# Optimization experiments

Hardware: AMD Instinct MI355X
Metric: run time of the kernel (lower is better)

The kernel has to match this reference:

```python
import jax, jax.numpy as jnp
import numpy as np

N, T, F = 4096, 10, 512
NHID, NCLASS = 64, 16


def setup_inputs() -> dict:
    key = jax.random.key(0)
    k1, k2, k3, k4, k5, k6 = jax.random.split(key, 6)
    feats = jax.random.normal(k1, (N, T, F), dtype=jnp.float32)
    adj = jax.random.uniform(k2, (T, N, N), dtype=jnp.float32)
    # GCNConv parameters (glorot-ish scale)
    W1 = jax.random.normal(k3, (F, NHID), dtype=jnp.float32) * (1.0 / np.sqrt(F))
    b1 = jnp.zeros((NHID,), dtype=jnp.float32)
    W2 = jax.random.normal(k4, (NHID, NCLASS), dtype=jnp.float32) * (1.0 / np.sqrt(NHID))
    b2 = jnp.zeros((NCLASS,), dtype=jnp.float32)
    lam = jnp.float32(0.2)
    return {"feats": feats, "adj": adj, "lam": lam,
            "W1": W1, "b1": b1, "W2": W2, "b2": b2}


def _fold_adj(adj, lam):
    # tf.foldl: prev = adj[0]; prev = (1-lam)*prev + lam*adj[t] for t=1..T-1
    def step(prev, a):
        return (1.0 - lam) * prev + lam * a, None
    folded, _ = jax.lax.scan(step, adj[0], adj[1:])
    # '0 * lam +' term from the original (a no-op numerically, kept for fidelity)
    return 0.0 * lam + folded


def reference(feats, adj, lam, W1, b1, W2, b2):
    A = _fold_adj(adj, lam)                      # [N, N]
    x = feats[:, -1, :]                          # [N, F] last snapshot features
    # GCNConv 1: relu(A @ (X W1) + b1)
    h = jax.nn.relu(A @ (x @ W1) + b1)           # [N, NHID]
    # dropout is identity in eval mode (training=None)
    # GCNConv 2: softmax(A @ (H W2) + b2)
    logits = A @ (h @ W2) + b2                   # [N, NCLASS]
    return jax.nn.softmax(logits, axis=-1)
```

## Files before the change

### kernel.cpp

```cpp
#include <hip/hip_runtime.h>
#include <stdint.h>

#define NN 4096
#define TT 10
#define FF 512
#define NHID 64
#define NCLASS 16

#define G1_BM 128
#define G1_BK 64
#define G1_SPLITS 8
#define G2_BM 64
#define G2_BK 64
#define G2_SPLITS 16

__global__ void fold_k(const float4* __restrict__ adj, float4* __restrict__ A,
                       const float* __restrict__ lam_p) {
    const float lam = lam_p[0];
    const float w = 1.0f - lam;
    const int64_t slice = (int64_t)NN * NN / 4;
    const int64_t stride = (int64_t)gridDim.x * blockDim.x;
    for (int64_t i = (int64_t)blockIdx.x * blockDim.x + threadIdx.x; i < slice; i += stride) {
        float4 v = adj[i];
#pragma unroll
        for (int t = 1; t < TT; ++t) {
            float4 a = adj[(int64_t)t * slice + i];
            v.x = w * v.x + lam * a.x;
            v.y = w * v.y + lam * a.y;
            v.z = w * v.z + lam * a.z;
            v.w = w * v.w + lam * a.w;
        }
        A[i] = v;
    }
}

__global__ __launch_bounds__(64) void xw1_k(const float* __restrict__ feats,
                                            const float* __restrict__ W1,
                                            float* __restrict__ XW1T) {
    __shared__ float xs[FF];
    const int n = blockIdx.x;
    const int k = threadIdx.x;
    const float4* xr4 = (const float4*)(feats + ((int64_t)n * TT + (TT - 1)) * FF);
    float4* xs4 = (float4*)xs;
#pragma unroll
    for (int f = k; f < FF / 4; f += 64) xs4[f] = xr4[f];
    __syncthreads();
    float acc = 0.0f;
#pragma unroll 8
    for (int f = 0; f < FF; ++f) acc = fmaf(xs[f], W1[f * NHID + k], acc);
    XW1T[(int64_t)k * NN + n] = acc;
}

__global__ __launch_bounds__(256) void gemm1_k(const float* __restrict__ A,
                                               const float* __restrict__ XW1T,
                                               float* __restrict__ Y1P) {
    __shared__ float As[G1_BM][G1_BK + 4];
    __shared__ float Bs[NHID][G1_BK + 4];
    const int t = threadIdx.x;
    const int r0 = blockIdx.y * G1_BM;
    const int s = blockIdx.x;
    const int jbase = s * (NN / G1_SPLITS);
    const int tr = t >> 4;
    const int tc = t & 15;

    float acc[8][4];
#pragma unroll
    for (int r = 0; r < 8; ++r)
#pragma unroll
        for (int c = 0; c < 4; ++c) acc[r][c] = 0.0f;

    for (int tile = 0; tile < (NN / G1_SPLITS) / G1_BK; ++tile) {
        const int j0 = jbase + tile * G1_BK;
#pragma unroll
        for (int u = 0; u < 8; ++u) {
            int idx = t + u * 256;
            int row = idx >> 4;
            int c4 = idx & 15;
            float4 v = *(const float4*)(A + (int64_t)(r0 + row) * NN + j0 + c4 * 4);
            *(float4*)&As[row][c4 * 4] = v;
        }
#pragma unroll
        for (int u = 0; u < 4; ++u) {
            int idx = t + u * 256;
            int row = idx >> 4;
            int c4 = idx & 15;
            float4 v = *(const float4*)(XW1T + (int64_t)row * NN + j0 + c4 * 4);
            *(float4*)&Bs[row][c4 * 4] = v;
        }
        __syncthreads();
#pragma unroll 2
        for (int kk = 0; kk < G1_BK; kk += 4) {
            float4 a[8], b[4];
#pragma unroll
            for (int r = 0; r < 8; ++r) a[r] = *(const float4*)&As[r * 16 + tr][kk];
#pragma unroll
            for (int c = 0; c < 4; ++c) b[c] = *(const float4*)&Bs[c * 16 + tc][kk];
#pragma unroll
            for (int r = 0; r < 8; ++r)
#pragma unroll
                for (int c = 0; c < 4; ++c) {
                    float v = acc[r][c];
                    v = fmaf(a[r].x, b[c].x, v);
                    v = fmaf(a[r].y, b[c].y, v);
                    v = fmaf(a[r].z, b[c].z, v);
                    v = fmaf(a[r].w, b[c].w, v);
                    acc[r][c] = v;
                }
        }
        __syncthreads();
    }
    float* out = Y1P + (int64_t)s * NN * NHID;
#pragma unroll
    for (int r = 0; r < 8; ++r) {
        int n = r0 + r * 16 + tr;
#pragma unroll
        for (int c = 0; c < 4; ++c) out[(int64_t)n * NHID + c * 16 + tc] = acc[r][c];
    }
}

__global__ __launch_bounds__(256) void hw2_k(const float* __restrict__ Y1P,
                                             const float* __restrict__ b1,
                                             const float* __restrict__ W2,
                                             float* __restrict__ HW2T) {
    __shared__ float hs[4][NHID];
    const int row = threadIdx.x >> 6;
    const int k = threadIdx.x & 63;
    const int n = blockIdx.x * 4 + row;
    float v = b1[k];
#pragma unroll
    for (int s = 0; s < G1_SPLITS; ++s)
        v += Y1P[(int64_t)s * NN * NHID + (int64_t)n * NHID + k];
    hs[row][k] = fmaxf(v, 0.0f);
    __syncthreads();
    if (k < NCLASS) {
        float acc = 0.0f;
#pragma unroll
        for (int j = 0; j < NHID; ++j) acc = fmaf(hs[row][j], W2[j * NCLASS + k], acc);
        HW2T[(int64_t)k * NN + n] = acc;
    }
}

__global__ __launch_bounds__(64) void gemm2_k(const float* __restrict__ A,
                                              const float* __restrict__ HW2T,
                                              float* __restrict__ LP) {
    __shared__ float As[G2_BM][G2_BK + 4];
    __shared__ float Bs[NCLASS][G2_BK + 4];
    const int t = threadIdx.x;
    const int r0 = blockIdx.y * G2_BM;
    const int s = blockIdx.x;
    const int jbase = s * (NN / G2_SPLITS);
    const int tr = t >> 2;
    const int tc = t & 3;

    float acc[4][4];
#pragma unroll
    for (int r = 0; r < 4; ++r)
#pragma unroll
        for (int c = 0; c < 4; ++c) acc[r][c] = 0.0f;

    for (int tile = 0; tile < (NN / G2_SPLITS) / G2_BK; ++tile) {
        const int j0 = jbase + tile * G2_BK;
#pragma unroll
        for (int u = 0; u < 16; ++u) {
            int idx = t + u * 64;
            int row = idx >> 4;
            int c4 = idx & 15;
            *(float4*)&As[row][c4 * 4] =
                *(const float4*)(A + (int64_t)(r0 + row) * NN + j0 + c4 * 4);
        }
#pragma unroll
        for (int u = 0; u < 4; ++u) {
            int idx = t + u * 64;
            int row = idx >> 4;
            int c4 = idx & 15;
            *(float4*)&Bs[row][c4 * 4] =
                *(const float4*)(HW2T + (int64_t)row * NN + j0 + c4 * 4);
        }
        __syncthreads();
#pragma unroll 2
        for (int kk = 0; kk < G2_BK; kk += 4) {
            float4 a[4], b[4];
#pragma unroll
            for (int r = 0; r < 4; ++r) a[r] = *(const float4*)&As[r * 16 + tr][kk];
#pragma unroll
            for (int c = 0; c < 4; ++c) b[c] = *(const float4*)&Bs[c * 4 + tc][kk];
#pragma unroll
            for (int r = 0; r < 4; ++r)
#pragma unroll
                for (int c = 0; c < 4; ++c) {
                    float v = acc[r][c];
                    v = fmaf(a[r].x, b[c].x, v);
                    v = fmaf(a[r].y, b[c].y, v);
                    v = fmaf(a[r].z, b[c].z, v);
                    v = fmaf(a[r].w, b[c].w, v);
                    acc[r][c] = v;
                }
        }
        __syncthreads();
    }
    float* out = LP + (int64_t)s * NN * NCLASS;
#pragma unroll
    for (int r = 0; r < 4; ++r) {
        int n = r0 + r * 16 + tr;
#pragma unroll
        for (int c = 0; c < 4; ++c) out[(int64_t)n * NCLASS + c * 4 + tc] = acc[r][c];
    }
}

__global__ __launch_bounds__(256) void softmax_k(const float* __restrict__ LP,
                                                 const float* __restrict__ b2,
                                                 float* __restrict__ outp) {
    const int n = blockIdx.x * blockDim.x + threadIdx.x;
    float l[NCLASS];
#pragma unroll
    for (int c = 0; c < NCLASS; ++c) l[c] = b2[c];
#pragma unroll
    for (int s = 0; s < G2_SPLITS; ++s) {
        const float4* p = (const float4*)(LP + (int64_t)s * NN * NCLASS + (int64_t)n * NCLASS);
#pragma unroll
        for (int q = 0; q < 4; ++q) {
            float4 v = p[q];
            l[q * 4 + 0] += v.x;
            l[q * 4 + 1] += v.y;
            l[q * 4 + 2] += v.z;
            l[q * 4 + 3] += v.w;
        }
    }
    float m = l[0];
#pragma unroll
    for (int c = 1; c < NCLASS; ++c) m = fmaxf(m, l[c]);
    float sum = 0.0f;
#pragma unroll
    for (int c = 0; c < NCLASS; ++c) {
        l[c] = __expf(l[c] - m);
        sum += l[c];
    }
    float inv = 1.0f / sum;
    float4* o = (float4*)(outp + (int64_t)n * NCLASS);
#pragma unroll
    for (int q = 0; q < 4; ++q)
        o[q] = make_float4(l[q * 4 + 0] * inv, l[q * 4 + 1] * inv, l[q * 4 + 2] * inv,
                           l[q * 4 + 3] * inv);
}

extern "C" void kernel_launch(void* const* d_in, const int* in_sizes, int n_in,
                              void* d_out, int out_size, void* d_ws, size_t ws_size,
                              hipStream_t stream) {
    const float* feats = (const float*)d_in[0];
    const float* adj = (const float*)d_in[1];
    const float* lam = (const float*)d_in[2];
    const float* W1 = (const float*)d_in[3];
    const float* b1 = (const float*)d_in[4];
    const float* W2 = (const float*)d_in[5];
    const float* b2 = (const float*)d_in[6];
    float* out = (float*)d_out;

    float* ws = (float*)d_ws;
    float* A = ws;
    float* XW1T = A + (int64_t)NN * NN;
    float* Y1P = XW1T + (int64_t)NHID * NN;
    float* HW2T = Y1P + (int64_t)G1_SPLITS * NN * NHID;
    float* LP = HW2T + (int64_t)NCLASS * NN;

    fold_k<<<4096, 256, 0, stream>>>((const float4*)adj, (float4*)A, lam);
    xw1_k<<<NN, 64, 0, stream>>>(feats, W1, XW1T);
    gemm1_k<<<dim3(G1_SPLITS, NN / G1_BM), 256, 0, stream>>>(A, XW1T, Y1P);
    hw2_k<<<NN / 4, 256, 0, stream>>>(Y1P, b1, W2, HW2T);
    gemm2_k<<<dim3(G2_SPLITS, NN / G2_BM), 64, 0, stream>>>(A, HW2T, LP);
    softmax_k<<<NN / 256, 256, 0, stream>>>(LP, b2, out);
}
```

Measured before the change: 1.005 ms.

## Fuse adjacency fold into first GEMM and retile xw1 and gemm2 kernels

The temporal fold of the adjacency slices now happens inside the first aggregation GEMM. Each tile is blended from the ten slices on load, placed in shared memory, and written once to global A for the second GEMM. This removes the separate fold pass and the re-read of A by gemm1. xw1 now computes 16 rows per 256-thread block to reuse W1 loads, and gemm2 moves to 256-thread blocks with 128-row tiles. The gemm1 split count doubles, which enlarges the partial-sum workspace. The fold loop now has only two loads unrolled per thread, which may limit memory-level parallelism on the dominant adjacency stream.

```diff
diff --git a/kernel.cpp b/kernel.cpp
--- a/kernel.cpp
+++ b/kernel.cpp
@@ -9,59 +9,55 @@
 
 #define G1_BM 128
 #define G1_BK 64
-#define G1_SPLITS 8
-#define G2_BM 64
+#define G1_SPLITS 16
+#define G2_BM 128
 #define G2_BK 64
 #define G2_SPLITS 16
 
-__global__ void fold_k(const float4* __restrict__ adj, float4* __restrict__ A,
-                       const float* __restrict__ lam_p) {
+__global__ __launch_bounds__(256) void xw1_k(const float* __restrict__ feats,
+                                             const float* __restrict__ W1,
+                                             float* __restrict__ XW1T) {
+    __shared__ float xs[16][FF];
+    const int t = threadIdx.x;
+    const int n0 = blockIdx.x * 16;
+#pragma unroll
+    for (int u = 0; u < 8; ++u) {
+        int idx = t + u * 256;
+        int row = idx >> 7;
+        int c4 = idx & 127;
+        ((float4*)xs[row])[c4] =
+            ((const float4*)(feats + ((int64_t)(n0 + row) * TT + (TT - 1)) * FF))[c4];
+    }
+    __syncthreads();
+    const int k = t & 63;
+    const int rl = t >> 6;
+    float acc[4] = {0.0f, 0.0f, 0.0f, 0.0f};
+#pragma unroll 8
+    for (int f = 0; f < FF; ++f) {
+        float wv = W1[f * NHID + k];
+#pragma unroll
+        for (int r = 0; r < 4; ++r) acc[r] = fmaf(xs[rl * 4 + r][f], wv, acc[r]);
+    }
+#pragma unroll
+    for (int r = 0; r < 4; ++r) XW1T[(int64_t)k * NN + n0 + rl * 4 + r] = acc[r];
+}
+
+__global__ __launch_bounds__(256) void foldgemm1_k(const float* __restrict__ adj,
+                                                   const float* __restrict__ lam_p,
+                                                   const float* __restrict__ XW1T,
+                                                   float* __restrict__ A,
+                                                   float* __restrict__ Y1P) {
+    __shared__ float As[G1_BM][G1_BK + 4];
+    __shared__ float Bs[NHID][G1_BK + 4];
     const float lam = lam_p[0];
     const float w = 1.0f - lam;
-    const int64_t slice = (int64_t)NN * NN / 4;
-    const int64_t stride = (int64_t)gridDim.x * blockDim.x;
-    for (int64_t i = (int64_t)blockIdx.x * blockDim.x + threadIdx.x; i < slice; i += stride) {
-        float4 v = adj[i];
-#pragma unroll
-        for (int t = 1; t < TT; ++t) {
-            float4 a = adj[(int64_t)t * slice + i];
-            v.x = w * v.x + lam * a.x;
-            v.y = w * v.y + lam * a.y;
-            v.z = w * v.z + lam * a.z;
-            v.w = w * v.w + lam * a.w;
-        }
-        A[i] = v;
-    }
-}
-
-__global__ __launch_bounds__(64) void xw1_k(const float* __restrict__ feats,
-                                            const float* __restrict__ W1,
-                                            float* __restrict__ XW1T) {
-    __shared__ float xs[FF];
-    const int n = blockIdx.x;
-    const int k = threadIdx.x;
-    const float4* xr4 = (const float4*)(feats + ((int64_t)n * TT + (TT - 1)) * FF);
-    float4* xs4 = (float4*)xs;
-#pragma unroll
-    for (int f = k; f < FF / 4; f += 64) xs4[f] = xr4[f];
-    __syncthreads();
-    float acc = 0.0f;
-#pragma unroll 8
-    for (int f = 0; f < FF; ++f) acc = fmaf(xs[f], W1[f * NHID + k], acc);
-    XW1T[(int64_t)k * NN + n] = acc;
-}
-
-__global__ __launch_bounds__(256) void gemm1_k(const float* __restrict__ A,
-                                               const float* __restrict__ XW1T,
-                                               float* __restrict__ Y1P) {
-    __shared__ float As[G1_BM][G1_BK + 4];
-    __shared__ float Bs[NHID][G1_BK + 4];
     const int t = threadIdx.x;
     const int r0 = blockIdx.y * G1_BM;
     const int s = blockIdx.x;
     const int jbase = s * (NN / G1_SPLITS);
     const int tr = t >> 4;
     const int tc = t & 15;
+    const int64_t slice = (int64_t)NN * NN;
 
     float acc[8][4];
 #pragma unroll
@@ -71,21 +67,31 @@
 
     for (int tile = 0; tile < (NN / G1_SPLITS) / G1_BK; ++tile) {
         const int j0 = jbase + tile * G1_BK;
-#pragma unroll
+#pragma unroll 2
         for (int u = 0; u < 8; ++u) {
             int idx = t + u * 256;
             int row = idx >> 4;
             int c4 = idx & 15;
-            float4 v = *(const float4*)(A + (int64_t)(r0 + row) * NN + j0 + c4 * 4);
+            const float* p = adj + (int64_t)(r0 + row) * NN + j0 + c4 * 4;
+            float4 v = *(const float4*)p;
+#pragma unroll
+            for (int tt = 1; tt < TT; ++tt) {
+                float4 a = *(const float4*)(p + (int64_t)tt * slice);
+                v.x = fmaf(lam, a.x, w * v.x);
+                v.y = fmaf(lam, a.y, w * v.y);
+                v.z = fmaf(lam, a.z, w * v.z);
+                v.w = fmaf(lam, a.w, w * v.w);
+            }
             *(float4*)&As[row][c4 * 4] = v;
+            *(float4*)(A + (int64_t)(r0 + row) * NN + j0 + c4 * 4) = v;
         }
 #pragma unroll
         for (int u = 0; u < 4; ++u) {
             int idx = t + u * 256;
             int row = idx >> 4;
             int c4 = idx & 15;
-            float4 v = *(const float4*)(XW1T + (int64_t)row * NN + j0 + c4 * 4);
-            *(float4*)&Bs[row][c4 * 4] = v;
+            *(float4*)&Bs[row][c4 * 4] =
+                *(const float4*)(XW1T + (int64_t)row * NN + j0 + c4 * 4);
         }
         __syncthreads();
 #pragma unroll 2
@@ -140,54 +146,52 @@
     }
 }
 
-__global__ __launch_bounds__(64) void gemm2_k(const float* __restrict__ A,
-                                              const float* __restrict__ HW2T,
-                                              float* __restrict__ LP) {
+__global__ __launch_bounds__(256) void gemm2_k(const float* __restrict__ A,
+                                               const float* __restrict__ HW2T,
+                                               float* __restrict__ LP) {
     __shared__ float As[G2_BM][G2_BK + 4];
     __shared__ float Bs[NCLASS][G2_BK + 4];
     const int t = threadIdx.x;
     const int r0 = blockIdx.y * G2_BM;
     const int s = blockIdx.x;
     const int jbase = s * (NN / G2_SPLITS);
-    const int tr = t >> 2;
-    const int tc = t & 3;
-
-    float acc[4][4];
+    const int tr = t >> 3;
+    const int tc = t & 7;
+
+    float acc[4][2];
 #pragma unroll
     for (int r = 0; r < 4; ++r)
 #pragma unroll
-        for (int c = 0; c < 4; ++c) acc[r][c] = 0.0f;
+        for (int c = 0; c < 2; ++c) acc[r][c] = 0.0f;
 
     for (int tile = 0; tile < (NN / G2_SPLITS) / G2_BK; ++tile) {
         const int j0 = jbase + tile * G2_BK;
 #pragma unroll
-        for (int u = 0; u < 16; ++u) {
-            int idx = t + u * 64;
+        for (int u = 0; u < 8; ++u) {
+            int idx = t + u * 256;
             int row = idx >> 4;
             int c4 = idx & 15;
             *(float4*)&As[row][c4 * 4] =
                 *(const float4*)(A + (int64_t)(r0 + row) * NN + j0 + c4 * 4);
         }
-#pragma unroll
-        for (int u = 0; u < 4; ++u) {
-            int idx = t + u * 64;
-            int row = idx >> 4;
-            int c4 = idx & 15;
+        {
+            int row = t >> 4;
+            int c4 = t & 15;
             *(float4*)&Bs[row][c4 * 4] =
                 *(const float4*)(HW2T + (int64_t)row * NN + j0 + c4 * 4);
         }
         __syncthreads();
 #pragma unroll 2
         for (int kk = 0; kk < G2_BK; kk += 4) {
-            float4 a[4], b[4];
-#pragma unroll
-            for (int r = 0; r < 4; ++r) a[r] = *(const float4*)&As[r * 16 + tr][kk];
-#pragma unroll
-            for (int c = 0; c < 4; ++c) b[c] = *(const float4*)&Bs[c * 4 + tc][kk];
+            float4 a[4], b[2];
+#pragma unroll
+            for (int r = 0; r < 4; ++r) a[r] = *(const float4*)&As[r * 32 + tr][kk];
+#pragma unroll
+            for (int c = 0; c < 2; ++c) b[c] = *(const float4*)&Bs[c * 8 + tc][kk];
 #pragma unroll
             for (int r = 0; r < 4; ++r)
 #pragma unroll
-                for (int c = 0; c < 4; ++c) {
+                for (int c = 0; c < 2; ++c) {
                     float v = acc[r][c];
                     v = fmaf(a[r].x, b[c].x, v);
                     v = fmaf(a[r].y, b[c].y, v);
@@ -201,9 +205,9 @@
     float* out = LP + (int64_t)s * NN * NCLASS;
 #pragma unroll
     for (int r = 0; r < 4; ++r) {
-        int n = r0 + r * 16 + tr;
-#pragma unroll
-        for (int c = 0; c < 4; ++c) out[(int64_t)n * NCLASS + c * 4 + tc] = acc[r][c];
+        int n = r0 + r * 32 + tr;
+#pragma unroll
+        for (int c = 0; c < 2; ++c) out[(int64_t)n * NCLASS + c * 8 + tc] = acc[r][c];
     }
 }
 
@@ -262,10 +266,9 @@
     float* HW2T = Y1P + (int64_t)G1_SPLITS * NN * NHID;
     float* LP = HW2T + (int64_t)NCLASS * NN;
 
-    fold_k<<<4096, 256, 0, stream>>>((const float4*)adj, (float4*)A, lam);
-    xw1_k<<<NN, 64, 0, stream>>>(feats, W1, XW1T);
-    gemm1_k<<<dim3(G1_SPLITS, NN / G1_BM), 256, 0, stream>>>(A, XW1T, Y1P);
+    xw1_k<<<NN / 16, 256, 0, stream>>>(feats, W1, XW1T);
+    foldgemm1_k<<<dim3(G1_SPLITS, NN / G1_BM), 256, 0, stream>>>(adj, lam, XW1T, A, Y1P);
     hw2_k<<<NN / 4, 256, 0, stream>>>(Y1P, b1, W2, HW2T);
-    gemm2_k<<<dim3(G2_SPLITS, NN / G2_BM), 64, 0, stream>>>(A, HW2T, LP);
+    gemm2_k<<<dim3(G2_SPLITS, NN / G2_BM), 256, 0, stream>>>(A, HW2T, LP);
     softmax_k<<<NN / 256, 256, 0, stream>>>(LP, b2, out);
 }
```

Result: faster. 969.8 us (-3.5%).
